# Kernel tuning notes

Measured on AMD Instinct MI355X. Metric: run time of the kernel, lower is better.

## Reference

```python
import jax, jax.numpy as jnp
import numpy as np

L = 12      # n_blocks
H = 12      # n_heads
V = 64      # val_dim
D = 768     # hidden_d (token dim)
MLP = 3072  # MLP_dim
NP = 14     # n_patches per side
PS = 16     # patch size
C = 3       # channels
NC = 1000   # num_classes
EPS = 1e-5  # LayerNorm eps


def pos_embeddings(S, d):
    # result[i,j] = sin(i/10000**(j/d)) if j even else cos(i/10000**((j-1)/d))
    i = jnp.arange(S, dtype=jnp.float32)[:, None]
    j = jnp.arange(d, dtype=jnp.float32)[None, :]
    angle = i / jnp.power(10000.0, (j - (j % 2)) / d)
    even = (jnp.arange(d) % 2) == 0
    return jnp.where(even[None, :], jnp.sin(angle), jnp.cos(angle))


def patchify(images):
    # [n,C,H,W] -> [n, NP*NP, C*PS*PS], patch flattened in (c, ph, pw) order
    n = images.shape[0]
    x = images.reshape(n, C, NP, PS, NP, PS)
    x = x.transpose(0, 2, 4, 1, 3, 5)  # n, i, j, c, ps, ps
    return x.reshape(n, NP * NP, C * PS * PS)


def layernorm(x, w, b):
    m = jnp.mean(x, axis=-1, keepdims=True)
    v = jnp.var(x, axis=-1, keepdims=True)
    return (x - m) * jax.lax.rsqrt(v + EPS) * w + b


def setup_inputs() -> dict:
    key = jax.random.key(0)
    ks = jax.random.split(key, 10)
    s = lambda k, shape, scale=0.02: jax.random.normal(k, shape, jnp.float32) * scale
    return {
        "images": jax.random.normal(ks[0], (32, C, NP * PS, NP * PS), jnp.float32),
        "W_map": s(ks[1], (C * PS * PS, D)),          # linear_mapper (no bias)
        "class_token": s(ks[2], (1, D), 1.0),
        "pos_emb": pos_embeddings(NP * NP + 1, D),     # buffer
        "ln1_w": jnp.ones((L, D)), "ln1_b": jnp.zeros((L, D)),
        "qkv_w": s(ks[3], (L, D, 3 * H * V)),          # to_qkv (no bias)
        "merge_w": s(ks[4], (L, H * V, D)),            # Merge (no bias)
        "ln2_w": jnp.ones((L, D)), "ln2_b": jnp.zeros((L, D)),
        "mlp_w1": s(ks[5], (L, D, MLP)), "mlp_b1": jnp.zeros((L, MLP)),
        "mlp_w2": s(ks[6], (L, MLP, D)), "mlp_b2": jnp.zeros((L, D)),
        "head_w": s(ks[7], (D, NC)), "head_b": jnp.zeros((NC,)),
    }


def reference(images, W_map, class_token, pos_emb, ln1_w, ln1_b, qkv_w,
              merge_w, ln2_w, ln2_b, mlp_w1, mlp_b1, mlp_w2, mlp_b2,
              head_w, head_b):
    n = images.shape[0]
    tokens = patchify(images) @ W_map                              # [n, P, D]
    tokens = jnp.concatenate([jnp.broadcast_to(class_token, (n, 1, D)), tokens], axis=1)
    x = tokens + pos_emb                                           # [n, P+1, D]

    def block(x, p):
        l1w, l1b, qw, mw, l2w, l2b, w1, b1, w2, b2 = p
        h = layernorm(x, l1w, l1b)
        # rearrange 'b p (h v k) -> k b h p v' (k innermost factor)
        qkv = (h @ qw).reshape(n, -1, H, V, 3)
        q, k, v = qkv[..., 0], qkv[..., 1], qkv[..., 2]            # [n, P+1, H, V]
        attn = jnp.einsum('bihd,bjhd->bhij', q, k) * (V ** -0.5)
        attn = jax.nn.softmax(attn, axis=-1)
        o = jnp.einsum('bhij,bjhd->bihd', attn, v).reshape(n, -1, H * V)
        x = x + o @ mw
        h2 = layernorm(x, l2w, l2b)
        x = x + (jax.nn.gelu(h2 @ w1 + b1, approximate=False) @ w2 + b2)
        return x, None

    x, _ = jax.lax.scan(block, x, (ln1_w, ln1_b, qkv_w, merge_w,
                                   ln2_w, ln2_b, mlp_w1, mlp_b1, mlp_w2, mlp_b2))
    return jax.nn.softmax(x[:, 0] @ head_w + head_b, axis=-1)      # [n, NC]
```

## Files before the change

### kernel.cpp

```cpp
#include <hip/hip_runtime.h>
#include <math.h>

#define NIMG 32
#define NP2  196
#define PTOK 197
#define DIM  768
#define NH   12
#define VD   64
#define MLPD 3072
#define ROWS (NIMG*PTOK)
#define PROWS (NIMG*NP2)
#define MPAD 6400
#define PSTR 208
#define BHN (NIMG*NH)

typedef float f32x4 __attribute__((ext_vector_type(4)));
typedef short bf16x8 __attribute__((ext_vector_type(8)));
typedef unsigned short u16x8 __attribute__((ext_vector_type(8)));
typedef unsigned short u16x4 __attribute__((ext_vector_type(4)));

__device__ __forceinline__ unsigned short f2bf(float x) {
    unsigned int u = __float_as_uint(x);
    return (unsigned short)((u + 0x7FFFu + ((u >> 16) & 1u)) >> 16);
}
__device__ __forceinline__ float bfhi(unsigned short h) {
    return __uint_as_float(((unsigned int)h) << 16);
}
__device__ __forceinline__ void glds16(const unsigned short* g, unsigned short* l) {
    __builtin_amdgcn_global_load_lds(
        (const __attribute__((address_space(1))) unsigned int*)g,
        (__attribute__((address_space(3))) unsigned int*)l, 16, 0, 0);
}

__global__ __launch_bounds__(256) void patchify_kernel(const float* __restrict__ img,
                                                       unsigned short* __restrict__ ph,
                                                       unsigned short* __restrict__ pl)
{
    int idx = blockIdx.x * 256 + threadIdx.x;
    if (idx >= PROWS * DIM) return;
    int row = idx / DIM, kk = idx % DIM;
    int b = row / NP2, p = row % NP2;
    int i = p / 14, j = p % 14;
    int c = kk >> 8, r = kk & 255;
    int pr = r >> 4, pw = r & 15;
    float v = img[(((size_t)b*3 + c)*224 + i*16 + pr)*224 + j*16 + pw];
    unsigned short hi = f2bf(v);
    ph[idx] = hi;
    pl[idx] = f2bf(v - bfhi(hi));
}

__global__ __launch_bounds__(256) void class_pos_kernel(const float* __restrict__ ct,
                                                        const float* __restrict__ pos,
                                                        float* __restrict__ x)
{
    int idx = blockIdx.x * 256 + threadIdx.x;
    if (idx >= NIMG * DIM) return;
    int b = idx / DIM, d = idx % DIM;
    x[(size_t)b * PTOK * DIM + d] = ct[d] + pos[d];
}

__device__ __forceinline__ void conv_body(const float* __restrict__ W,
    unsigned short* __restrict__ Bh, unsigned short* __restrict__ Bl, int K, int N)
{
    int idx = blockIdx.x * 256 + threadIdx.x;
    if (idx >= N * (K >> 5)) return;
    int kb = idx / N;
    int n  = idx - kb * N;
    size_t off = (((size_t)(n >> 7) * (K >> 5) + kb) * 128 + (n & 127)) * 32;
    #pragma unroll
    for (int u = 0; u < 4; ++u) {
        u16x8 h, l;
        #pragma unroll
        for (int j = 0; j < 8; ++j) {
            float x = W[(size_t)(kb * 32 + u * 8 + j) * N + n];
            unsigned short hh = f2bf(x);
            h[j] = hh;
            l[j] = f2bf(x - bfhi(hh));
        }
        *(u16x8*)&Bh[off + u * 8] = h;
        *(u16x8*)&Bl[off + u * 8] = l;
    }
}

__global__ __launch_bounds__(256) void convert_one(const float* __restrict__ W,
    unsigned short* __restrict__ Bh, unsigned short* __restrict__ Bl, int K, int N)
{
    conv_body(W, Bh, Bl, K, N);
}

__global__ __launch_bounds__(256) void convert_layer(
    const float* __restrict__ qw, const float* __restrict__ mw,
    const float* __restrict__ w1, const float* __restrict__ w2,
    unsigned short* qh, unsigned short* ql, unsigned short* mh, unsigned short* ml,
    unsigned short* h1, unsigned short* l1, unsigned short* h2, unsigned short* l2)
{
    switch (blockIdx.y) {
        case 0: conv_body(qw, qh, ql, DIM, 3*NH*VD); break;
        case 1: conv_body(mw, mh, ml, DIM, DIM);     break;
        case 2: conv_body(w1, h1, l1, DIM, MLPD);    break;
        case 3: conv_body(w2, h2, l2, MLPD, DIM);    break;
    }
}

template<int MODE>
__device__ __forceinline__ void epi_store(
    int r, int c, float val, float* __restrict__ C, int M, int N,
    const float* __restrict__ bias, const float* __restrict__ res,
    const float* __restrict__ pos,
    unsigned int* __restrict__ qo, unsigned int* __restrict__ ko, unsigned int* __restrict__ vo,
    unsigned short* __restrict__ oph, unsigned short* __restrict__ opl)
{
    if (MODE == 1) {
        int b = r / NP2, p = r - b * NP2;
        C[((size_t)b * PTOK + 1 + p) * DIM + c] = val + pos[(size_t)(p + 1) * DIM + c];
    } else if (MODE == 2) {
        int b = r / PTOK, p = r - b * PTOK;
        int t = c % 3, hv = c / 3;
        int hd = hv >> 6, vv = hv & 63;
        size_t bh = (size_t)b * NH + hd;
        float sv = (t == 0) ? val * 0.125f : val;
        unsigned short hi = f2bf(sv);
        unsigned short lo = f2bf(sv - bfhi(hi));
        unsigned int w32 = (unsigned int)hi | ((unsigned int)lo << 16);
        if (t == 2) vo[(bh * 64 + vv) * PSTR + p] = w32;
        else if (t == 0) qo[(bh * PSTR + p) * 64 + vv] = w32;
        else ko[(bh * PSTR + p) * 64 + vv] = w32;
    } else if (MODE == 3) {
        float tmp = val + bias[c];
        float gel = 0.5f * tmp * (1.0f + erff(tmp * 0.70710678118654752f));
        unsigned short hi = f2bf(gel);
        oph[(size_t)r * N + c] = hi;
        opl[(size_t)r * N + c] = f2bf(gel - bfhi(hi));
    } else if (MODE == 4) {
        C[(size_t)r * N + c] = res[(size_t)r * N + c] + val;
    } else if (MODE == 5) {
        C[(size_t)r * N + c] = res[(size_t)r * N + c] + val + bias[c];
    }
}

template<int MODE>
__global__ __launch_bounds__(256, 4) void mgemm(
    const unsigned short* __restrict__ Ah, const unsigned short* __restrict__ Al,
    const unsigned short* __restrict__ Bh, const unsigned short* __restrict__ Bl,
    float* __restrict__ C, int M, int N, int K, int gm, int gn,
    const float* __restrict__ bias, const float* __restrict__ res,
    const float* __restrict__ pos,
    unsigned int* __restrict__ qo, unsigned int* __restrict__ ko, unsigned int* __restrict__ vo,
    unsigned short* __restrict__ oph, unsigned short* __restrict__ opl)
{
    __shared__ unsigned short SAh[4096];
    __shared__ unsigned short SAl[4096];
    __shared__ unsigned short SBh[4096];
    __shared__ unsigned short SBl[4096];

    const int tid = threadIdx.x;
    const int nwg = gm * gn;
    const int q = nwg >> 3, r = nwg & 7;
    const int xcd = blockIdx.x & 7, li = blockIdx.x >> 3;
    const int seq = xcd * q + (xcd < r ? xcd : r) + li;
    const int mt = seq / gn, nt = seq - mt * gn;
    const int m0 = mt * 128, n0 = nt * 128;

    const int wave = tid >> 6, lane = tid & 63;
    const int wm = (wave >> 1) * 64, wn = (wave & 1) * 64;
    const int lr = lane & 15, lg = lane >> 4;

    const int r0 = tid >> 2, sl = tid & 3;
    const int s0 = sl ^ ((r0 >> 1) & 3);
    const size_t aoff0 = (size_t)(m0 + r0) * K + s0 * 8;
    const size_t aoff1 = (size_t)(m0 + r0 + 64) * K + s0 * 8;
    const size_t boff0 = (size_t)(n0 >> 7) * (K >> 5) * 4096 + (size_t)r0 * 32 + s0 * 8;

    int aro[4], bro[4];
    #pragma unroll
    for (int i = 0; i < 4; ++i) {
        int rowA = wm + i * 16 + lr;
        aro[i] = rowA * 32 + ((lg ^ ((rowA >> 1) & 3)) * 8);
        int rowB = wn + i * 16 + lr;
        bro[i] = rowB * 32 + ((lg ^ ((rowB >> 1) & 3)) * 8);
    }

    f32x4 acc[4][4];
    #pragma unroll
    for (int i = 0; i < 4; ++i)
        #pragma unroll
        for (int j = 0; j < 4; ++j)
            #pragma unroll
            for (int e = 0; e < 4; ++e) acc[i][j][e] = 0.f;

    const int kSteps = K >> 5;
    #pragma unroll 1
    for (int ks = 0; ks < kSteps; ++ks) {
        __syncthreads();
        const size_t ak = (size_t)ks * 32;
        const size_t bk = (size_t)ks * 4096;
        glds16(Ah + aoff0 + ak, SAh + tid * 8);
        glds16(Ah + aoff1 + ak, SAh + 2048 + tid * 8);
        glds16(Al + aoff0 + ak, SAl + tid * 8);
        glds16(Al + aoff1 + ak, SAl + 2048 + tid * 8);
        glds16(Bh + boff0 + bk, SBh + tid * 8);
        glds16(Bh + boff0 + bk + 2048, SBh + 2048 + tid * 8);
        glds16(Bl + boff0 + bk, SBl + tid * 8);
        glds16(Bl + boff0 + bk + 2048, SBl + 2048 + tid * 8);
        __syncthreads();

        bf16x8 bfh[4], bfl[4];
        #pragma unroll
        for (int ni = 0; ni < 4; ++ni) {
            bfh[ni] = *(const bf16x8*)&SBh[bro[ni]];
            bfl[ni] = *(const bf16x8*)&SBl[bro[ni]];
        }
        #pragma unroll
        for (int mi = 0; mi < 4; ++mi) {
            bf16x8 afh = *(const bf16x8*)&SAh[aro[mi]];
            bf16x8 afl = *(const bf16x8*)&SAl[aro[mi]];
            #pragma unroll
            for (int ni = 0; ni < 4; ++ni) {
                acc[mi][ni] = __builtin_amdgcn_mfma_f32_16x16x32_bf16(afh, bfh[ni], acc[mi][ni], 0, 0, 0);
                acc[mi][ni] = __builtin_amdgcn_mfma_f32_16x16x32_bf16(afh, bfl[ni], acc[mi][ni], 0, 0, 0);
                acc[mi][ni] = __builtin_amdgcn_mfma_f32_16x16x32_bf16(afl, bfh[ni], acc[mi][ni], 0, 0, 0);
            }
        }
    }

    #pragma unroll
    for (int mi = 0; mi < 4; ++mi) {
        #pragma unroll
        for (int ni = 0; ni < 4; ++ni) {
            f32x4 v = acc[mi][ni];
            int c = n0 + wn + ni * 16 + lr;
            #pragma unroll
            for (int rr = 0; rr < 4; ++rr) {
                int rr2 = m0 + wm + mi * 16 + lg * 4 + rr;
                if (rr2 >= M) continue;
                epi_store<MODE>(rr2, c, v[rr], C, M, N, bias, res, pos, qo, ko, vo, oph, opl);
            }
        }
    }
}

template<int MODE>
__global__ __launch_bounds__(512, 2) void mgemm2(
    const unsigned short* __restrict__ Ah, const unsigned short* __restrict__ Al,
    const unsigned short* __restrict__ Bh, const unsigned short* __restrict__ Bl,
    float* __restrict__ C, int M, int N, int K, int gm, int gn,
    const float* __restrict__ bias, const float* __restrict__ res,
    const float* __restrict__ pos,
    unsigned int* __restrict__ qo, unsigned int* __restrict__ ko, unsigned int* __restrict__ vo,
    unsigned short* __restrict__ oph, unsigned short* __restrict__ opl)
{
    __shared__ unsigned short SAh[2 * 8192];
    __shared__ unsigned short SAl[2 * 8192];
    __shared__ unsigned short SBh[2 * 8192];
    __shared__ unsigned short SBl[2 * 8192];

    const int tid = threadIdx.x;
    const int nwg = gm * gn;
    const int q = nwg >> 3, r = nwg & 7;
    const int xcd = blockIdx.x & 7, li = blockIdx.x >> 3;
    const int seq = xcd * q + (xcd < r ? xcd : r) + li;
    const int mt = seq / gn, nt = seq - mt * gn;
    const int m0 = mt * 256, n0 = nt * 256;

    const int wave = tid >> 6, lane = tid & 63;
    const int wm = (wave >> 2) * 128, wn = (wave & 3) * 64;
    const int lr = lane & 15, lg = lane >> 4;

    const int r0 = tid >> 2, sl = tid & 3;
    const int s0 = sl ^ ((r0 >> 1) & 3);
    const size_t aoff0 = (size_t)(m0 + r0) * K + s0 * 8;
    const size_t aoff1 = (size_t)(m0 + r0 + 128) * K + s0 * 8;
    const size_t bstep = (size_t)(K >> 5) * 4096;
    const size_t bo0 = (size_t)(n0 >> 7) * bstep + (size_t)r0 * 32 + s0 * 8;
    const size_t bo1 = bo0 + bstep;

    int aro[8], bro[4];
    #pragma unroll
    for (int i = 0; i < 8; ++i) {
        int rowA = wm + i * 16 + lr;
        aro[i] = rowA * 32 + ((lg ^ ((rowA >> 1) & 3)) * 8);
    }
    #pragma unroll
    for (int i = 0; i < 4; ++i) {
        int rowB = wn + i * 16 + lr;
        bro[i] = rowB * 32 + ((lg ^ ((rowB >> 1) & 3)) * 8);
    }

    f32x4 acc[8][4];
    #pragma unroll
    for (int i = 0; i < 8; ++i)
        #pragma unroll
        for (int j = 0; j < 4; ++j)
            #pragma unroll
            for (int e = 0; e < 4; ++e) acc[i][j][e] = 0.f;

#define STAGE2(KS, B) do { \
    const size_t _ak = (size_t)(KS) * 32; \
    const size_t _bk = (size_t)(KS) * 4096; \
    unsigned short* _sah = SAh + (B) * 8192; \
    unsigned short* _sal = SAl + (B) * 8192; \
    unsigned short* _sbh = SBh + (B) * 8192; \
    unsigned short* _sbl = SBl + (B) * 8192; \
    glds16(Ah + aoff0 + _ak, _sah + tid * 8); \
    glds16(Ah + aoff1 + _ak, _sah + 4096 + tid * 8); \
    glds16(Al + aoff0 + _ak, _sal + tid * 8); \
    glds16(Al + aoff1 + _ak, _sal + 4096 + tid * 8); \
    glds16(Bh + bo0 + _bk, _sbh + tid * 8); \
    glds16(Bh + bo1 + _bk, _sbh + 4096 + tid * 8); \
    glds16(Bl + bo0 + _bk, _sbl + tid * 8); \
    glds16(Bl + bo1 + _bk, _sbl + 4096 + tid * 8); \
} while (0)

#define COMPUTE2(B) do { \
    const unsigned short* _sah = SAh + (B) * 8192; \
    const unsigned short* _sal = SAl + (B) * 8192; \
    const unsigned short* _sbh = SBh + (B) * 8192; \
    const unsigned short* _sbl = SBl + (B) * 8192; \
    bf16x8 bfh[4], bfl[4]; \
    _Pragma("unroll") \
    for (int ni = 0; ni < 4; ++ni) { \
        bfh[ni] = *(const bf16x8*)&_sbh[bro[ni]]; \
        bfl[ni] = *(const bf16x8*)&_sbl[bro[ni]]; \
    } \
    _Pragma("unroll") \
    for (int mi = 0; mi < 8; ++mi) { \
        bf16x8 afh = *(const bf16x8*)&_sah[aro[mi]]; \
        bf16x8 afl = *(const bf16x8*)&_sal[aro[mi]]; \
        _Pragma("unroll") \
        for (int ni = 0; ni < 4; ++ni) { \
            acc[mi][ni] = __builtin_amdgcn_mfma_f32_16x16x32_bf16(afh, bfh[ni], acc[mi][ni], 0, 0, 0); \
            acc[mi][ni] = __builtin_amdgcn_mfma_f32_16x16x32_bf16(afh, bfl[ni], acc[mi][ni], 0, 0, 0); \
            acc[mi][ni] = __builtin_amdgcn_mfma_f32_16x16x32_bf16(afl, bfh[ni], acc[mi][ni], 0, 0, 0); \
        } \
    } \
} while (0)

#define WAITBAR2 do { \
    asm volatile("s_waitcnt vmcnt(0)" ::: "memory"); \
    __builtin_amdgcn_s_barrier(); \
} while (0)

    const int kSteps = K >> 5;
    STAGE2(0, 0);
    WAITBAR2;

    #pragma unroll 1
    for (int ks = 0; ks < kSteps; ks += 2) {
        STAGE2(ks + 1, 1);
        COMPUTE2(0);
        WAITBAR2;
        if (ks + 2 < kSteps) STAGE2(ks + 2, 0);
        COMPUTE2(1);
        WAITBAR2;
    }
#undef STAGE2
#undef COMPUTE2
#undef WAITBAR2

    #pragma unroll
    for (int mi = 0; mi < 8; ++mi) {
        #pragma unroll
        for (int ni = 0; ni < 4; ++ni) {
            f32x4 v = acc[mi][ni];
            int c = n0 + wn + ni * 16 + lr;
            #pragma unroll
            for (int rr = 0; rr < 4; ++rr) {
                int rr2 = m0 + wm + mi * 16 + lg * 4 + rr;
                if (rr2 >= M) continue;
                epi_store<MODE>(rr2, c, v[rr], C, M, N, bias, res, pos, qo, ko, vo, oph, opl);
            }
        }
    }
}

__global__ __launch_bounds__(256) void ln_kernel(const float* __restrict__ x,
                                                 const float* __restrict__ w,
                                                 const float* __restrict__ b,
                                                 unsigned short* __restrict__ oh,
                                                 unsigned short* __restrict__ ol, int rows)
{
    int wave = threadIdx.x >> 6, lane = threadIdx.x & 63;
    int row = blockIdx.x * 4 + wave;
    if (row >= rows) return;
    const float* xr = x + (size_t)row * DIM;
    float vals[12];
    float sum = 0.f;
    #pragma unroll
    for (int u = 0; u < 12; ++u) { vals[u] = xr[u * 64 + lane]; sum += vals[u]; }
    #pragma unroll
    for (int off = 32; off; off >>= 1) sum += __shfl_xor(sum, off);
    float mean = sum * (1.f / DIM);
    float vs = 0.f;
    #pragma unroll
    for (int u = 0; u < 12; ++u) { float d = vals[u] - mean; vs += d * d; }
    #pragma unroll
    for (int off = 32; off; off >>= 1) vs += __shfl_xor(vs, off);
    float rstd = rsqrtf(vs * (1.f / DIM) + 1e-5f);
    #pragma unroll
    for (int u = 0; u < 12; ++u) {
        int d = u * 64 + lane;
        float v = (vals[u] - mean) * rstd * w[d] + b[d];
        unsigned short hi = f2bf(v);
        oh[(size_t)row * DIM + d] = hi;
        ol[(size_t)row * DIM + d] = f2bf(v - bfhi(hi));
    }
}

__global__ __launch_bounds__(256) void attn_mfma(
    const unsigned int* __restrict__ qp, const unsigned int* __restrict__ kp,
    const unsigned int* __restrict__ vtp,
    unsigned short* __restrict__ oh, unsigned short* __restrict__ ol)
{
    __shared__ unsigned short KVh[64 * 72];
    __shared__ unsigned short KVl[64 * 72];
    __shared__ unsigned short Ph[64 * 72];
    __shared__ unsigned short Pl[64 * 72];

    const int tid = threadIdx.x;
    const int w = tid >> 6, lane = tid & 63;
    const int l = lane & 15, g = lane >> 4;
    const int bh = blockIdx.y, q0 = blockIdx.x * 64;
    const int b = bh / NH, hd = bh - b * NH;

    int qrow = q0 + 16 * w + l;
    if (qrow >= PTOK) qrow = 0;
    const unsigned int* qbase = qp + ((size_t)bh * PSTR + qrow) * 64;
    bf16x8 qAh[2], qAl[2];
    #pragma unroll
    for (int ks = 0; ks < 2; ++ks) {
        const unsigned int* p = qbase + 32 * ks + 8 * g;
        uint4 a = *(const uint4*)p;
        uint4 c = *(const uint4*)(p + 4);
        bf16x8 h8, l8;
        h8[0]=(short)a.x; h8[1]=(short)a.y; h8[2]=(short)a.z; h8[3]=(short)a.w;
        h8[4]=(short)c.x; h8[5]=(short)c.y; h8[6]=(short)c.z; h8[7]=(short)c.w;
        l8[0]=(short)(a.x>>16); l8[1]=(short)(a.y>>16); l8[2]=(short)(a.z>>16); l8[3]=(short)(a.w>>16);
        l8[4]=(short)(c.x>>16); l8[5]=(short)(c.y>>16); l8[6]=(short)(c.z>>16); l8[7]=(short)(c.w>>16);
        qAh[ks] = h8; qAl[ks] = l8;
    }

    f32x4 s[13];
    #pragma unroll
    for (int t = 0; t < 13; ++t)
        #pragma unroll
        for (int e = 0; e < 4; ++e) s[t][e] = 0.f;

    for (int c = 0; c < 4; ++c) {
        __syncthreads();
        const int rows = (c < 3) ? 64 : 16;
        for (int u = tid; u < rows * 16; u += 256) {
            int r = u >> 4, cc = u & 15;
            int j = c * 64 + r;
            uint4 wv = make_uint4(0, 0, 0, 0);
            if (j < PTOK) wv = *(const uint4*)(kp + ((size_t)bh * PSTR + j) * 64 + cc * 4);
            u16x4 h4, l4;
            h4[0]=(unsigned short)wv.x; h4[1]=(unsigned short)wv.y;
            h4[2]=(unsigned short)wv.z; h4[3]=(unsigned short)wv.w;
            l4[0]=(unsigned short)(wv.x>>16); l4[1]=(unsigned short)(wv.y>>16);
            l4[2]=(unsigned short)(wv.z>>16); l4[3]=(unsigned short)(wv.w>>16);
            *(u16x4*)&KVh[r * 72 + cc * 4] = h4;
            *(u16x4*)&KVl[r * 72 + cc * 4] = l4;
        }
        __syncthreads();
        const int tc = (c < 3) ? 4 : 1;
        for (int t = 0; t < tc; ++t) {
            int ti = c * 4 + t;
            #pragma unroll
            for (int ks = 0; ks < 2; ++ks) {
                bf16x8 kh = *(const bf16x8*)&KVh[(16 * t + l) * 72 + 32 * ks + 8 * g];
                bf16x8 kl = *(const bf16x8*)&KVl[(16 * t + l) * 72 + 32 * ks + 8 * g];
                s[ti] = __builtin_amdgcn_mfma_f32_16x16x32_bf16(qAh[ks], kh, s[ti], 0, 0, 0);
                s[ti] = __builtin_amdgcn_mfma_f32_16x16x32_bf16(qAh[ks], kl, s[ti], 0, 0, 0);
                s[ti] = __builtin_amdgcn_mfma_f32_16x16x32_bf16(qAl[ks], kh, s[ti], 0, 0, 0);
            }
        }
    }

    if (l >= 5) {
        #pragma unroll
        for (int e = 0; e < 4; ++e) s[12][e] = -1e30f;
    }

    float mx[4], rs[4];
    #pragma unroll
    for (int e = 0; e < 4; ++e) {
        float m = s[0][e];
        #pragma unroll
        for (int t = 1; t < 13; ++t) m = fmaxf(m, s[t][e]);
        #pragma unroll
        for (int off = 1; off < 16; off <<= 1) m = fmaxf(m, __shfl_xor(m, off));
        mx[e] = m;
    }
    #pragma unroll
    for (int e = 0; e < 4; ++e) {
        float sum = 0.f;
        #pragma unroll
        for (int t = 0; t < 13; ++t) {
            float p = __expf(s[t][e] - mx[e]);
            s[t][e] = p;
            sum += p;
        }
        #pragma unroll
        for (int off = 1; off < 16; off <<= 1) sum += __shfl_xor(sum, off);
        rs[e] = 1.f / sum;
    }

    f32x4 o[4];
    #pragma unroll
    for (int t = 0; t < 4; ++t)
        #pragma unroll
        for (int e = 0; e < 4; ++e) o[t][e] = 0.f;

    for (int c = 0; c < 4; ++c) {
        __syncthreads();
        const int cols = (c < 3) ? 64 : 32;
        const int cpr = cols >> 2;
        for (int u = tid; u < 64 * cpr; u += 256) {
            int r = u / cpr, cc = u % cpr;
            int jbase = c * 64 + cc * 4;
            uint4 wv;
            if (c < 3) {
                wv = *(const uint4*)(vtp + ((size_t)bh * 64 + r) * PSTR + jbase);
            } else {
                unsigned int t0 = (jbase + 0 < PTOK) ? vtp[((size_t)bh * 64 + r) * PSTR + jbase + 0] : 0u;
                unsigned int t1 = (jbase + 1 < PTOK) ? vtp[((size_t)bh * 64 + r) * PSTR + jbase + 1] : 0u;
                unsigned int t2 = (jbase + 2 < PTOK) ? vtp[((size_t)bh * 64 + r) * PSTR + jbase + 2] : 0u;
                unsigned int t3 = (jbase + 3 < PTOK) ? vtp[((size_t)bh * 64 + r) * PSTR + jbase + 3] : 0u;
                wv = make_uint4(t0, t1, t2, t3);
            }
            u16x4 h4, l4;
            h4[0]=(unsigned short)wv.x; h4[1]=(unsigned short)wv.y;
            h4[2]=(unsigned short)wv.z; h4[3]=(unsigned short)wv.w;
            l4[0]=(unsigned short)(wv.x>>16); l4[1]=(unsigned short)(wv.y>>16);
            l4[2]=(unsigned short)(wv.z>>16); l4[3]=(unsigned short)(wv.w>>16);
            *(u16x4*)&KVh[r * 72 + cc * 4] = h4;
            *(u16x4*)&KVl[r * 72 + cc * 4] = l4;
        }
        const int tc = (c < 3) ? 4 : 1;
        for (int t = 0; t < tc; ++t) {
            int ti = c * 4 + t;
            #pragma unroll
            for (int e = 0; e < 4; ++e) {
                int row = 16 * w + 4 * g + e, col = 16 * t + l;
                float pv = s[ti][e];
                unsigned short hi = f2bf(pv);
                Ph[row * 72 + col] = hi;
                Pl[row * 72 + col] = f2bf(pv - bfhi(hi));
            }
        }
        __syncthreads();
        const int ksn = (c < 3) ? 2 : 1;
        for (int ks = 0; ks < ksn; ++ks) {
            bf16x8 pa_h = *(const bf16x8*)&Ph[(16 * w + l) * 72 + 32 * ks + 8 * g];
            bf16x8 pa_l = *(const bf16x8*)&Pl[(16 * w + l) * 72 + 32 * ks + 8 * g];
            #pragma unroll
            for (int tv = 0; tv < 4; ++tv) {
                bf16x8 vh = *(const bf16x8*)&KVh[(16 * tv + l) * 72 + 32 * ks + 8 * g];
                bf16x8 vl = *(const bf16x8*)&KVl[(16 * tv + l) * 72 + 32 * ks + 8 * g];
                o[tv] = __builtin_amdgcn_mfma_f32_16x16x32_bf16(pa_h, vh, o[tv], 0, 0, 0);
                o[tv] = __builtin_amdgcn_mfma_f32_16x16x32_bf16(pa_h, vl, o[tv], 0, 0, 0);
                o[tv] = __builtin_amdgcn_mfma_f32_16x16x32_bf16(pa_l, vh, o[tv], 0, 0, 0);
            }
        }
    }

    #pragma unroll
    for (int tv = 0; tv < 4; ++tv) {
        #pragma unroll
        for (int e = 0; e < 4; ++e) {
            int q = q0 + 16 * w + 4 * g + e;
            if (q < PTOK) {
                float v = o[tv][e] * rs[e];
                size_t idx = ((size_t)(b * PTOK + q)) * DIM + hd * 64 + 16 * tv + l;
                unsigned short hi = f2bf(v);
                oh[idx] = hi;
                ol[idx] = f2bf(v - bfhi(hi));
            }
        }
    }
}

__global__ __launch_bounds__(256) void head_kernel(const float* __restrict__ x,
                                                   const float* __restrict__ W,
                                                   const float* __restrict__ bias,
                                                   float* __restrict__ out)
{
    __shared__ __align__(16) float xl[DIM];
    __shared__ float red[4];
    int b = blockIdx.x;
    const float* xr = x + (size_t)b * PTOK * DIM;
    for (int idx = threadIdx.x; idx < DIM; idx += 256) xl[idx] = xr[idx];
    __syncthreads();

    float logit[4];
    #pragma unroll
    for (int u = 0; u < 4; ++u) {
        int c = threadIdx.x + u * 256;
        float acc = (c < 1000) ? bias[c] : -INFINITY;
        if (c < 1000) {
            for (int k = 0; k < DIM; k += 4) {
                float4 xv = *(const float4*)&xl[k];
                acc += xv.x * W[(size_t)k * 1000 + c]
                     + xv.y * W[(size_t)(k + 1) * 1000 + c]
                     + xv.z * W[(size_t)(k + 2) * 1000 + c]
                     + xv.w * W[(size_t)(k + 3) * 1000 + c];
            }
        }
        logit[u] = acc;
    }
    int lane = threadIdx.x & 63, wv = threadIdx.x >> 6;
    float m = fmaxf(fmaxf(logit[0], logit[1]), fmaxf(logit[2], logit[3]));
    #pragma unroll
    for (int off = 32; off; off >>= 1) m = fmaxf(m, __shfl_xor(m, off));
    if (lane == 0) red[wv] = m;
    __syncthreads();
    m = fmaxf(fmaxf(red[0], red[1]), fmaxf(red[2], red[3]));

    float p[4]; float sum = 0.f;
    #pragma unroll
    for (int u = 0; u < 4; ++u) {
        int c = threadIdx.x + u * 256;
        p[u] = (c < 1000) ? expf(logit[u] - m) : 0.f;
        sum += p[u];
    }
    #pragma unroll
    for (int off = 32; off; off >>= 1) sum += __shfl_xor(sum, off);
    __syncthreads();
    if (lane == 0) red[wv] = sum;
    __syncthreads();
    float inv = 1.f / (red[0] + red[1] + red[2] + red[3]);
    #pragma unroll
    for (int u = 0; u < 4; ++u) {
        int c = threadIdx.x + u * 256;
        if (c < 1000) out[(size_t)b * 1000 + c] = p[u] * inv;
    }
}

extern "C" void kernel_launch(void* const* d_in, const int* in_sizes, int n_in,
                              void* d_out, int out_size, void* d_ws, size_t ws_size,
                              hipStream_t stream)
{
    const float* images  = (const float*)d_in[0];
    const float* W_map   = (const float*)d_in[1];
    const float* ct      = (const float*)d_in[2];
    const float* pos     = (const float*)d_in[3];
    const float* ln1_w   = (const float*)d_in[4];
    const float* ln1_b   = (const float*)d_in[5];
    const float* qkv_w   = (const float*)d_in[6];
    const float* merge_w = (const float*)d_in[7];
    const float* ln2_w   = (const float*)d_in[8];
    const float* ln2_b   = (const float*)d_in[9];
    const float* mlp_w1  = (const float*)d_in[10];
    const float* mlp_b1  = (const float*)d_in[11];
    const float* mlp_w2  = (const float*)d_in[12];
    const float* mlp_b2  = (const float*)d_in[13];
    const float* head_w  = (const float*)d_in[14];
    const float* head_b  = (const float*)d_in[15];
    float* out = (float*)d_out;

    float* ws = (float*)d_ws;
    const size_t XE   = (size_t)ROWS * DIM;
    const size_t PLND = (size_t)MPAD * DIM;
    const size_t GPL  = (size_t)MPAD * MLPD;

    float* x = ws;
    unsigned short* hh = (unsigned short*)(x + XE);
    unsigned short* hl = hh + PLND;
    unsigned short* oh = hl + PLND;
    unsigned short* ol = oh + PLND;
    unsigned short* gh = ol + PLND;
    unsigned short* gl = gh + GPL;

    const size_t PL = (size_t)BHN * PSTR * 64;
    unsigned int* qpl = (unsigned int*)gh;
    unsigned int* kpl = qpl + PL;
    unsigned int* vtp = kpl + PL;
    unsigned short* pph = gh;
    unsigned short* ppl = pph + PLND;

    unsigned short* wb = gl + GPL;
    const size_t qkvE = (size_t)DIM * 2304;
    const size_t mgE  = (size_t)DIM * DIM;
    const size_t m1E  = (size_t)DIM * MLPD;
    const size_t m2E  = (size_t)MLPD * DIM;
    unsigned short* qh  = wb;
    unsigned short* ql  = qh  + qkvE;
    unsigned short* mh  = ql  + qkvE;
    unsigned short* ml  = mh  + mgE;
    unsigned short* h1  = ml  + mgE;
    unsigned short* l1  = h1  + m1E;
    unsigned short* h2  = l1  + m1E;
    unsigned short* l2  = h2  + m2E;
    unsigned short* wmh = l2  + m2E;
    unsigned short* wml = wmh + mgE;

    patchify_kernel<<<(PROWS * DIM + 255) / 256, 256, 0, stream>>>(images, pph, ppl);
    class_pos_kernel<<<(NIMG * DIM + 255) / 256, 256, 0, stream>>>(ct, pos, x);
    convert_one<<<(DIM * (DIM / 32) + 255) / 256, 256, 0, stream>>>(W_map, wmh, wml, DIM, DIM);

    const int gme = 49;
    mgemm<1><<<gme * 6, 256, 0, stream>>>(
        pph, ppl, wmh, wml, x, PROWS, DIM, DIM, gme, 6,
        nullptr, nullptr, pos, nullptr, nullptr, nullptr, nullptr, nullptr);

    const int gm = 50;
    const int gm2 = 25;
    for (int l = 0; l < 12; ++l) {
        convert_layer<<<dim3(288, 4), 256, 0, stream>>>(
            qkv_w + (size_t)l * qkvE, merge_w + (size_t)l * mgE,
            mlp_w1 + (size_t)l * m1E, mlp_w2 + (size_t)l * m2E,
            qh, ql, mh, ml, h1, l1, h2, l2);
        ln_kernel<<<(ROWS + 3) / 4, 256, 0, stream>>>(x, ln1_w + l * DIM, ln1_b + l * DIM, hh, hl, ROWS);
        mgemm2<2><<<gm2 * 9, 512, 0, stream>>>(
            hh, hl, qh, ql, nullptr, ROWS, 2304, DIM, gm2, 9,
            nullptr, nullptr, nullptr, qpl, kpl, vtp, nullptr, nullptr);
        attn_mfma<<<dim3(4, BHN), 256, 0, stream>>>(qpl, kpl, vtp, oh, ol);
        mgemm<4><<<gm * 6, 256, 0, stream>>>(
            oh, ol, mh, ml, x, ROWS, DIM, DIM, gm, 6,
            nullptr, x, nullptr, nullptr, nullptr, nullptr, nullptr, nullptr);
        ln_kernel<<<(ROWS + 3) / 4, 256, 0, stream>>>(x, ln2_w + l * DIM, ln2_b + l * DIM, hh, hl, ROWS);
        mgemm2<3><<<gm2 * 12, 512, 0, stream>>>(
            hh, hl, h1, l1, nullptr, ROWS, MLPD, DIM, gm2, 12,
            mlp_b1 + (size_t)l * MLPD, nullptr, nullptr, nullptr, nullptr, nullptr, gh, gl);
        mgemm<5><<<gm * 6, 256, 0, stream>>>(
            gh, gl, h2, l2, x, ROWS, DIM, MLPD, gm, 6,
            mlp_b2 + (size_t)l * DIM, x, nullptr, nullptr, nullptr, nullptr, nullptr, nullptr);
    }
    head_kernel<<<NIMG, 256, 0, stream>>>(x, head_w, head_b, out);
}
```

Before: 6.182 ms.

## Single-buffer the 256x256 split-bf16 GEMM to raise occupancy

The 256x256 GEMM used for QKV and MLP-up drops its double-buffered LDS staging in favour of a single buffer loaded and consumed inside each K step between two barriers. LDS per block halves to 64KB and the launch bound asks for 4 waves per SIMD instead of 2, so the aim is to hide load latency through more resident blocks rather than software pipelining. The cost is that global-to-LDS loads no longer overlap the MFMA work within a block, and a register cap of 128 VGPRs against 128 accumulator floats per thread may cause spilling.

```diff
diff --git a/kernel.cpp b/kernel.cpp
--- a/kernel.cpp
+++ b/kernel.cpp
@@ -240,7 +240,7 @@
 }
 
 template<int MODE>
-__global__ __launch_bounds__(512, 2) void mgemm2(
+__global__ __launch_bounds__(512, 4) void mgemm2s(
     const unsigned short* __restrict__ Ah, const unsigned short* __restrict__ Al,
     const unsigned short* __restrict__ Bh, const unsigned short* __restrict__ Bl,
     float* __restrict__ C, int M, int N, int K, int gm, int gn,
@@ -249,10 +249,10 @@
     unsigned int* __restrict__ qo, unsigned int* __restrict__ ko, unsigned int* __restrict__ vo,
     unsigned short* __restrict__ oph, unsigned short* __restrict__ opl)
 {
-    __shared__ unsigned short SAh[2 * 8192];
-    __shared__ unsigned short SAl[2 * 8192];
-    __shared__ unsigned short SBh[2 * 8192];
-    __shared__ unsigned short SBl[2 * 8192];
+    __shared__ unsigned short SAh[8192];
+    __shared__ unsigned short SAl[8192];
+    __shared__ unsigned short SBh[8192];
+    __shared__ unsigned short SBl[8192];
 
     const int tid = threadIdx.x;
     const int nwg = gm * gn;
@@ -294,68 +294,40 @@
             #pragma unroll
             for (int e = 0; e < 4; ++e) acc[i][j][e] = 0.f;
 
-#define STAGE2(KS, B) do { \
-    const size_t _ak = (size_t)(KS) * 32; \
-    const size_t _bk = (size_t)(KS) * 4096; \
-    unsigned short* _sah = SAh + (B) * 8192; \
-    unsigned short* _sal = SAl + (B) * 8192; \
-    unsigned short* _sbh = SBh + (B) * 8192; \
-    unsigned short* _sbl = SBl + (B) * 8192; \
-    glds16(Ah + aoff0 + _ak, _sah + tid * 8); \
-    glds16(Ah + aoff1 + _ak, _sah + 4096 + tid * 8); \
-    glds16(Al + aoff0 + _ak, _sal + tid * 8); \
-    glds16(Al + aoff1 + _ak, _sal + 4096 + tid * 8); \
-    glds16(Bh + bo0 + _bk, _sbh + tid * 8); \
-    glds16(Bh + bo1 + _bk, _sbh + 4096 + tid * 8); \
-    glds16(Bl + bo0 + _bk, _sbl + tid * 8); \
-    glds16(Bl + bo1 + _bk, _sbl + 4096 + tid * 8); \
-} while (0)
-
-#define COMPUTE2(B) do { \
-    const unsigned short* _sah = SAh + (B) * 8192; \
-    const unsigned short* _sal = SAl + (B) * 8192; \
-    const unsigned short* _sbh = SBh + (B) * 8192; \
-    const unsigned short* _sbl = SBl + (B) * 8192; \
-    bf16x8 bfh[4], bfl[4]; \
-    _Pragma("unroll") \
-    for (int ni = 0; ni < 4; ++ni) { \
-        bfh[ni] = *(const bf16x8*)&_sbh[bro[ni]]; \
-        bfl[ni] = *(const bf16x8*)&_sbl[bro[ni]]; \
-    } \
-    _Pragma("unroll") \
-    for (int mi = 0; mi < 8; ++mi) { \
-        bf16x8 afh = *(const bf16x8*)&_sah[aro[mi]]; \
-        bf16x8 afl = *(const bf16x8*)&_sal[aro[mi]]; \
-        _Pragma("unroll") \
-        for (int ni = 0; ni < 4; ++ni) { \
-            acc[mi][ni] = __builtin_amdgcn_mfma_f32_16x16x32_bf16(afh, bfh[ni], acc[mi][ni], 0, 0, 0); \
-            acc[mi][ni] = __builtin_amdgcn_mfma_f32_16x16x32_bf16(afh, bfl[ni], acc[mi][ni], 0, 0, 0); \
-            acc[mi][ni] = __builtin_amdgcn_mfma_f32_16x16x32_bf16(afl, bfh[ni], acc[mi][ni], 0, 0, 0); \
-        } \
-    } \
-} while (0)
-
-#define WAITBAR2 do { \
-    asm volatile("s_waitcnt vmcnt(0)" ::: "memory"); \
-    __builtin_amdgcn_s_barrier(); \
-} while (0)
-
     const int kSteps = K >> 5;
-    STAGE2(0, 0);
-    WAITBAR2;
-
     #pragma unroll 1
-    for (int ks = 0; ks < kSteps; ks += 2) {
-        STAGE2(ks + 1, 1);
-        COMPUTE2(0);
-        WAITBAR2;
-        if (ks + 2 < kSteps) STAGE2(ks + 2, 0);
-        COMPUTE2(1);
-        WAITBAR2;
-    }
-#undef STAGE2
-#undef COMPUTE2
-#undef WAITBAR2
+    for (int ks = 0; ks < kSteps; ++ks) {
+        __syncthreads();
+        const size_t ak = (size_t)ks * 32;
+        const size_t bk = (size_t)ks * 4096;
+        glds16(Ah + aoff0 + ak, SAh + tid * 8);
+        glds16(Ah + aoff1 + ak, SAh + 4096 + tid * 8);
+        glds16(Al + aoff0 + ak, SAl + tid * 8);
+        glds16(Al + aoff1 + ak, SAl + 4096 + tid * 8);
+        glds16(Bh + bo0 + bk, SBh + tid * 8);
+        glds16(Bh + bo1 + bk, SBh + 4096 + tid * 8);
+        glds16(Bl + bo0 + bk, SBl + tid * 8);
+        glds16(Bl + bo1 + bk, SBl + 4096 + tid * 8);
+        __syncthreads();
+
+        bf16x8 bfh[4], bfl[4];
+        #pragma unroll
+        for (int ni = 0; ni < 4; ++ni) {
+            bfh[ni] = *(const bf16x8*)&SBh[bro[ni]];
+            bfl[ni] = *(const bf16x8*)&SBl[bro[ni]];
+        }
+        #pragma unroll
+        for (int mi = 0; mi < 8; ++mi) {
+            bf16x8 afh = *(const bf16x8*)&SAh[aro[mi]];
+            bf16x8 afl = *(const bf16x8*)&SAl[aro[mi]];
+            #pragma unroll
+            for (int ni = 0; ni < 4; ++ni) {
+                acc[mi][ni] = __builtin_amdgcn_mfma_f32_16x16x32_bf16(afh, bfh[ni], acc[mi][ni], 0, 0, 0);
+                acc[mi][ni] = __builtin_amdgcn_mfma_f32_16x16x32_bf16(afh, bfl[ni], acc[mi][ni], 0, 0, 0);
+                acc[mi][ni] = __builtin_amdgcn_mfma_f32_16x16x32_bf16(afl, bfh[ni], acc[mi][ni], 0, 0, 0);
+            }
+        }
+    }
 
     #pragma unroll
     for (int mi = 0; mi < 8; ++mi) {
@@ -711,7 +683,7 @@
             mlp_w1 + (size_t)l * m1E, mlp_w2 + (size_t)l * m2E,
             qh, ql, mh, ml, h1, l1, h2, l2);
         ln_kernel<<<(ROWS + 3) / 4, 256, 0, stream>>>(x, ln1_w + l * DIM, ln1_b + l * DIM, hh, hl, ROWS);
-        mgemm2<2><<<gm2 * 9, 512, 0, stream>>>(
+        mgemm2s<2><<<gm2 * 9, 512, 0, stream>>>(
             hh, hl, qh, ql, nullptr, ROWS, 2304, DIM, gm2, 9,
             nullptr, nullptr, nullptr, qpl, kpl, vtp, nullptr, nullptr);
         attn_mfma<<<dim3(4, BHN), 256, 0, stream>>>(qpl, kpl, vtp, oh, ol);
@@ -719,7 +691,7 @@
             oh, ol, mh, ml, x, ROWS, DIM, DIM, gm, 6,
             nullptr, x, nullptr, nullptr, nullptr, nullptr, nullptr, nullptr);
         ln_kernel<<<(ROWS + 3) / 4, 256, 0, stream>>>(x, ln2_w + l * DIM, ln2_b + l * DIM, hh, hl, ROWS);
-        mgemm2<3><<<gm2 * 12, 512, 0, stream>>>(
+        mgemm2s<3><<<gm2 * 12, 512, 0, stream>>>(
             hh, hl, h1, l1, nullptr, ROWS, MLPD, DIM, gm2, 12,
             mlp_b1 + (size_t)l * MLPD, nullptr, nullptr, nullptr, nullptr, nullptr, gh, gl);
         mgemm<5><<<gm * 6, 256, 0, stream>>>(
```

Measured after the change: 20.59 ms. +233.0%, slower.
